# Kernel optimization log

Hardware: AMD Instinct MI355X
Metric: run time of the kernel (lower is better)

## Reference

```python
import jax, jax.numpy as jnp
import numpy as np

B, T, C, H, D, S = 4096, 256, 64, 16, 16, 10


def setup_inputs() -> dict:
    key = jax.random.key(0)
    ks = jax.random.split(key, 8)
    return {
        'states_seq': jax.random.uniform(ks[0], (B, T, S), dtype=jnp.float32) + 0.5,
        'covariates_seq': jax.random.normal(ks[1], (B, T, C), dtype=jnp.float32),
        'ln_gamma': jnp.ones((C,), jnp.float32),
        'ln_beta': jnp.zeros((C,), jnp.float32),
        'rnn_wx': jax.random.normal(ks[2], (C, H), dtype=jnp.float32) * 0.1,
        'rnn_wh': jax.random.normal(ks[3], (H, H), dtype=jnp.float32) * 0.1,
        'rnn_b': jnp.zeros((H,), jnp.float32),
        'd1_w': jax.random.normal(ks[4], (H, H), dtype=jnp.float32) * 0.1,
        'd1_b': jnp.zeros((H,), jnp.float32),
        'd2_w': jax.random.normal(ks[5], (H, D), dtype=jnp.float32) * 0.1,
        'd2_b': jnp.zeros((D,), jnp.float32),
    }


def _cash_budget(s, d):
    # Deterministic cash-budget accounting update.
    # s: (B, 10) = [rev_prev, cash, AR, inventory, PPE, AP, debt, equity, retained, other]
    # d: (B, 16) drivers; first 10 used as ratios.
    sig = jax.nn.sigmoid
    g      = jnp.tanh(d[:, 0]) * 0.2      # sales growth
    cogs_m = sig(d[:, 1])                 # COGS margin
    opex_m = sig(d[:, 2]) * 0.5           # opex margin
    dep_r  = sig(d[:, 3]) * 0.1           # depreciation rate on PPE
    capex_r = sig(d[:, 4]) * 0.2          # capex as % of revenue
    dso = sig(d[:, 5])                    # AR ratio
    dio = sig(d[:, 6])                    # inventory ratio
    dpo = sig(d[:, 7])                    # AP ratio
    tax_r = sig(d[:, 8]) * 0.35           # tax rate
    int_r = sig(d[:, 9]) * 0.1            # interest rate on debt

    rev_prev, cash, ar, inv, ppe, ap, debt, equity, re, other = [s[:, i] for i in range(10)]
    rev = rev_prev * (1.0 + g)
    cogs = cogs_m * rev
    opex = opex_m * rev
    dep = dep_r * ppe
    interest = int_r * debt
    ebt = rev - cogs - opex - dep - interest
    tax = tax_r * jnp.maximum(ebt, 0.0)
    ni = ebt - tax
    ar_new = dso * rev
    inv_new = dio * cogs
    ap_new = dpo * cogs
    capex = capex_r * rev
    ppe_new = ppe + capex - dep
    cash_new = cash + ni + dep - capex - (ar_new - ar) - (inv_new - inv) + (ap_new - ap)
    re_new = re + ni
    s_next = jnp.stack([rev, cash_new, ar_new, inv_new, ppe_new, ap_new, debt, equity, re_new, other], axis=-1)
    is_out = jnp.stack([rev, cogs, opex, dep, interest, tax, ni], axis=-1)  # (B, 7)
    return s_next, is_out


def reference(states_seq, covariates_seq, ln_gamma, ln_beta, rnn_wx, rnn_wh, rnn_b, d1_w, d1_b, d2_w, d2_b):
    # LayerNormalization (keras default eps=1e-3, last axis)
    mu = covariates_seq.mean(-1, keepdims=True)
    var = covariates_seq.var(-1, keepdims=True)
    x = (covariates_seq - mu) * jax.lax.rsqrt(var + 1e-3) * ln_gamma + ln_beta

    # SimpleRNN: h_t = tanh(x_t Wx + h_{t-1} Wh + b), return_sequences
    xw = jnp.einsum('btc,ch->bth', x, rnn_wx) + rnn_b  # precompute input projection

    def rnn_step(h, xt):
        h = jnp.tanh(xt + h @ rnn_wh)
        return h, h

    h0 = jnp.zeros((x.shape[0], rnn_wh.shape[0]), x.dtype)
    _, hs = jax.lax.scan(rnn_step, h0, jnp.swapaxes(xw, 0, 1))  # (T, B, H)
    hs = jnp.swapaxes(hs, 0, 1)  # (B, T, H)

    drivers = jnp.tanh(hs @ d1_w + d1_b) @ d2_w + d2_b  # (B, T, D)

    # Cash-budget recurrence over t = 1 .. T-1
    def cb_step(s_prev, d_t):
        s_next, is_out = _cash_budget(s_prev, d_t)
        return s_next, (s_next, is_out)

    s0 = states_seq[:, 0, :]
    _, (states_tm, is_tm) = jax.lax.scan(cb_step, s0, jnp.swapaxes(drivers[:, 1:, :], 0, 1))
    states_pred = jnp.swapaxes(states_tm, 0, 1)  # (B, T-1, 10)
    is_pred = jnp.swapaxes(is_tm, 0, 1)          # (B, T-1, 7)
    return states_pred, is_pred
```

## Files before the change

### kernel.cpp

```cpp
#include <hip/hip_runtime.h>
#include <hip/hip_fp16.h>

#define NB 4096
#define NT 256
#define NC 64
#define NH 16
#define NS 10
#define NTO 255

__device__ __forceinline__ float fast_rcp(float x){ return __builtin_amdgcn_rcpf(x); }
__device__ __forceinline__ float fast_rsq(float x){ return __builtin_amdgcn_rsqf(x); }
__device__ __forceinline__ float fsig(float x){ return fast_rcp(1.0f + __expf(-x)); }
__device__ __forceinline__ float ftanh(float x){
    float e = __expf(2.0f*x);
    return fmaf(-2.0f, fast_rcp(e + 1.0f), 1.0f);
}

template<int R>
__device__ __forceinline__ float rotf(float x){
    return __int_as_float(__builtin_amdgcn_update_dpp(
        0, __float_as_int(x), 0x120 + R, 0xF, 0xF, true));
}
__device__ __forceinline__ float row_bcast_sum(float x){
    x += rotf<8>(x);
    x += rotf<4>(x);
    x += rotf<2>(x);
    x += rotf<1>(x);
    return x;
}

__global__ __launch_bounds__(256, 4) void xw_kernel(
    const float* __restrict__ cov, const float* __restrict__ lng,
    const float* __restrict__ lnb, const float* __restrict__ wx,
    const float* __restrict__ rnb, __half* __restrict__ xws)
{
    const int wid  = threadIdx.x >> 6;
    const int lane = threadIdx.x & 63;
    const int g = lane >> 4, l = lane & 15;
    const int b = (blockIdx.x << 2) + wid;

    float gwr[64];
    #pragma unroll
    for (int r = 0; r < 16; ++r) {
        int c0 = 4 * ((l - r) & 15);
        #pragma unroll
        for (int j = 0; j < 4; ++j)
            gwr[4*r+j] = lng[c0+j] * wx[(c0+j)*NH + l];
    }
    float bwb = rnb[l];
    #pragma unroll
    for (int c = 0; c < NC; ++c) bwb = fmaf(lnb[c], wx[c*NH + l], bwb);

    const float4* gp = (const float4*)cov + (size_t)b*NT*16 + g*16 + l;
    __half* op = xws + ((size_t)b*16 + l)*NT + g;

    float4 cur = gp[0];
    float4 nxt = gp[64];
    #pragma unroll 2
    for (int it = 0; it < 64; ++it) {
        float4 x = cur;
        cur = nxt;
        if (it < 62) nxt = gp[(size_t)(it+2)*64];
        float ss = (x.x + x.y) + (x.z + x.w);
        float sq = fmaf(x.x,x.x, fmaf(x.y,x.y, fmaf(x.z,x.z, x.w*x.w)));
        ss = row_bcast_sum(ss);
        sq = row_bcast_sum(sq);
        float mu  = ss * (1.0f/64.0f);
        float var = fmaf(-mu, mu, sq * (1.0f/64.0f));
        float rs  = fast_rsq(var + 0.001f);
        float nmu = -mu * rs;
        float x0 = fmaf(x.x, rs, nmu), x1 = fmaf(x.y, rs, nmu);
        float x2 = fmaf(x.z, rs, nmu), x3 = fmaf(x.w, rs, nmu);
        float a0 = bwb, a1 = 0.f, a2 = 0.f, a3 = 0.f;
        a0 = fmaf(x0, gwr[0], a0); a1 = fmaf(x1, gwr[1], a1);
        a2 = fmaf(x2, gwr[2], a2); a3 = fmaf(x3, gwr[3], a3);
#define ROTSTEP(R) { float r0=rotf<R>(x0), r1=rotf<R>(x1), r2=rotf<R>(x2), r3=rotf<R>(x3); \
        a0=fmaf(r0,gwr[4*R+0],a0); a1=fmaf(r1,gwr[4*R+1],a1); \
        a2=fmaf(r2,gwr[4*R+2],a2); a3=fmaf(r3,gwr[4*R+3],a3); }
        ROTSTEP(1)  ROTSTEP(2)  ROTSTEP(3)  ROTSTEP(4)  ROTSTEP(5)
        ROTSTEP(6)  ROTSTEP(7)  ROTSTEP(8)  ROTSTEP(9)  ROTSTEP(10)
        ROTSTEP(11) ROTSTEP(12) ROTSTEP(13) ROTSTEP(14) ROTSTEP(15)
#undef ROTSTEP
        float xw = (a0+a1)+(a2+a3);
        op[it*4] = __float2half(xw);
    }
}

__global__ __launch_bounds__(64, 1) void scan_kernel(
    const float* __restrict__ states, const __half* __restrict__ xws,
    const float* __restrict__ wh,     const float* __restrict__ d1w,
    const float* __restrict__ d1b,    const float* __restrict__ d2w,
    const float* __restrict__ d2b,    float* __restrict__ out)
{
    const int lane = threadIdx.x;
    const int g = lane >> 4, l = lane & 15;
    const int b = (blockIdx.x << 2) + g;

    __shared__ __align__(16) float db[8*64];

    float whr[NH], d1r[NH], d2r[NH];
    #pragma unroll
    for (int r = 0; r < NH; ++r) {
        int src = (l - r) & 15;
        whr[r] = wh[src*NH + l];
        d1r[r] = d1w[src*NH + l];
        d2r[r] = d2w[src*NH + l];
    }
    const float d1bl = d1b[l], d2bl = d2b[l];
    const float Aa = (l==0)?0.4f:(l==2)?0.5f:(l==3)?0.1f:(l==4)?0.2f:(l==8)?0.35f:(l==9)?0.1f:1.0f;
    const float Ba = (l==0)?2.0f:1.0f;
    const float Ca = (l==0)?-0.2f:0.0f;

    float s0,s1,s2,s3,s4,s5,s6,s7,s8,s9;
    { const float* sp = states + (size_t)b*NT*NS;
      s0=sp[0];s1=sp[1];s2=sp[2];s3=sp[3];s4=sp[4];
      s5=sp[5];s6=sp[6];s7=sp[7];s8=sp[8];s9=sp[9]; }

    float* spo = out + (size_t)b*NTO*NS + l;
    float* ipo = out + (size_t)NB*NTO*NS + (size_t)b*NTO*7 + l;

    const ushort4* xp = (const ushort4*)(xws + ((size_t)b*16 + l)*NT);
    ushort4 xa = xp[0], xb = xp[1];

    float h = 0.f;
    float t1p = 0.f;

#define XH(V,U) __half2float(__ushort_as_half((U)==0?(V).x:(U)==1?(V).y:(U)==2?(V).z:(V).w))

#define STEP(J, XWV, S1F, S2F, S3F, S4F) do { \
     \
    float4 w0{}, w1{}; float2 w2{}; \
    if (S4F) { const float* rb = db + ((((J)-3)&7)<<6) + (g<<4); \
        w0 = *(const float4*)rb; w1 = *(const float4*)(rb+4); w2 = *(const float2*)(rb+8); } \
    float hn = h, t1n = t1p; \
    float eR = 0.f, eD = 0.f, sR = 0.f, sD = 0.f; \
    if (S1F || S2F) { \
        float r1=rotf<1>(h),  r2=rotf<2>(h),  r3=rotf<3>(h),  r4=rotf<4>(h); \
        float r5=rotf<5>(h),  r6=rotf<6>(h),  r7=rotf<7>(h),  r8=rotf<8>(h); \
        float r9=rotf<9>(h),  r10=rotf<10>(h), r11=rotf<11>(h), r12=rotf<12>(h); \
        float r13=rotf<13>(h), r14=rotf<14>(h), r15=rotf<15>(h); \
        float aR0=(XWV), aR1=0.f, aR2=0.f, aR3=0.f; \
        float aD0=d1bl,  aD1=0.f, aD2=0.f, aD3=0.f; \
        if (S1F) aR0=fmaf(h,  whr[0], aR0);   if (S2F) aD0=fmaf(h,  d1r[0], aD0); \
        if (S1F) aR1=fmaf(r1, whr[1], aR1);   if (S2F) aD1=fmaf(r1, d1r[1], aD1); \
        if (S1F) aR2=fmaf(r2, whr[2], aR2);   if (S2F) aD2=fmaf(r2, d1r[2], aD2); \
        if (S1F) aR3=fmaf(r3, whr[3], aR3);   if (S2F) aD3=fmaf(r3, d1r[3], aD3); \
        if (S1F) aR0=fmaf(r4, whr[4], aR0);   if (S2F) aD0=fmaf(r4, d1r[4], aD0); \
        if (S1F) aR1=fmaf(r5, whr[5], aR1);   if (S2F) aD1=fmaf(r5, d1r[5], aD1); \
        if (S1F) aR2=fmaf(r6, whr[6], aR2);   if (S2F) aD2=fmaf(r6, d1r[6], aD2); \
        if (S1F) aR3=fmaf(r7, whr[7], aR3);   if (S2F) aD3=fmaf(r7, d1r[7], aD3); \
        if (S1F) aR0=fmaf(r8, whr[8], aR0);   if (S2F) aD0=fmaf(r8, d1r[8], aD0); \
        if (S1F) aR1=fmaf(r9, whr[9], aR1);   if (S2F) aD1=fmaf(r9, d1r[9], aD1); \
        if (S1F) aR2=fmaf(r10,whr[10],aR2);   if (S2F) aD2=fmaf(r10,d1r[10],aD2); \
        if (S1F) aR3=fmaf(r11,whr[11],aR3);   if (S2F) aD3=fmaf(r11,d1r[11],aD3); \
        if (S1F) aR0=fmaf(r12,whr[12],aR0);   if (S2F) aD0=fmaf(r12,d1r[12],aD0); \
        if (S1F) aR1=fmaf(r13,whr[13],aR1);   if (S2F) aD1=fmaf(r13,d1r[13],aD1); \
        if (S1F) aR2=fmaf(r14,whr[14],aR2);   if (S2F) aD2=fmaf(r14,d1r[14],aD2); \
        if (S1F) aR3=fmaf(r15,whr[15],aR3);   if (S2F) aD3=fmaf(r15,d1r[15],aD3); \
        if (S1F) sR = (aR0+aR1)+(aR2+aR3); \
        if (S2F) sD = (aD0+aD1)+(aD2+aD3); \
        if (S1F) eR = __expf(2.0f*sR); \
        if (S2F) eD = __expf(2.0f*sD); \
    } \
     \
    float dv = 0.f; \
    if (S3F) { \
        float q1=rotf<1>(t1p),  q2=rotf<2>(t1p),  q3=rotf<3>(t1p),  q4=rotf<4>(t1p); \
        float q5=rotf<5>(t1p),  q6=rotf<6>(t1p),  q7=rotf<7>(t1p),  q8=rotf<8>(t1p); \
        float q9=rotf<9>(t1p),  q10=rotf<10>(t1p), q11=rotf<11>(t1p), q12=rotf<12>(t1p); \
        float q13=rotf<13>(t1p), q14=rotf<14>(t1p), q15=rotf<15>(t1p); \
        float aS0=d2bl, aS1=0.f, aS2=0.f, aS3=0.f; \
        aS0=fmaf(t1p,d2r[0],aS0); aS1=fmaf(q1, d2r[1], aS1); \
        aS2=fmaf(q2, d2r[2], aS2); aS3=fmaf(q3, d2r[3], aS3); \
        aS0=fmaf(q4, d2r[4], aS0); aS1=fmaf(q5, d2r[5], aS1); \
        aS2=fmaf(q6, d2r[6], aS2); aS3=fmaf(q7, d2r[7], aS3); \
        aS0=fmaf(q8, d2r[8], aS0); aS1=fmaf(q9, d2r[9], aS1); \
        aS2=fmaf(q10,d2r[10],aS2); aS3=fmaf(q11,d2r[11],aS3); \
        aS0=fmaf(q12,d2r[12],aS0); aS1=fmaf(q13,d2r[13],aS1); \
        aS2=fmaf(q14,d2r[14],aS2); aS3=fmaf(q15,d2r[15],aS3); \
        dv = (aS0+aS1)+(aS2+aS3); \
    } \
     \
    if (S1F) hn  = fmaf(-2.0f, fast_rcp(eR+1.0f), 1.0f); \
    if (S2F) t1n = fmaf(-2.0f, fast_rcp(eD+1.0f), 1.0f); \
    if (S3F) { \
        float es = __expf(-Ba*dv); \
        float act = fmaf(Aa, fast_rcp(1.0f+es), Ca); \
        db[((((J)-2)&7)<<6) + lane] = act; \
    } \
    if (S4F) { \
        float rev   = fmaf(s0, w0.x, s0); \
        float cogs  = w0.y * rev; \
        float opex  = w0.z * rev; \
        float dep   = w0.w * s4; \
        float inte  = w2.y * s6; \
        float ebt   = (((rev - cogs) - opex) - dep) - inte; \
        float tax   = w2.x * fmaxf(ebt, 0.0f); \
        float ni    = ebt - tax; \
        float arn   = w1.y * rev; \
        float invn  = w1.z * cogs; \
        float apn   = w1.w * cogs; \
        float capex = w1.x * rev; \
        float ppen  = (s4 + capex) - dep; \
        float cashn = (((((s1 + ni) + dep) - capex) - (arn - s2)) - (invn - s3)) + (apn - s5); \
        float ren   = s8 + ni; \
        s0=rev; s1=cashn; s2=arn; s3=invn; s4=ppen; s5=apn; s8=ren; \
        float sv = (l==0)?rev:(l==1)?cashn:(l==2)?arn:(l==3)?invn:(l==4)?ppen: \
                   (l==5)?apn:(l==6)?s6:(l==7)?s7:(l==8)?ren:s9; \
        float iv = (l==0)?rev:(l==1)?cogs:(l==2)?opex:(l==3)?dep:(l==4)?inte:(l==5)?tax:ni; \
        if (l < NS) *spo = sv; \
        if (l < 7)  *ipo = iv; \
        spo += NS; ipo += 7; \
    } \
    h = hn; t1p = t1n; \
} while(0)

    {
        ushort4 xc = xa; xa = xb; xb = xp[2];
        h = ftanh(XH(xc,0));
        STEP(1, XH(xc,1), 1,0,0,0);
        STEP(2, XH(xc,2), 1,1,0,0);
        STEP(3, XH(xc,3), 1,1,1,0);
    }

    #pragma unroll 1
    for (int tt = 1; tt < 64; ++tt) {
        ushort4 xc = xa; xa = xb;
        if (tt < 62) xb = xp[tt+2];
        STEP(4*tt+0, XH(xc,0), 1,1,1,1);
        STEP(4*tt+1, XH(xc,1), 1,1,1,1);
        STEP(4*tt+2, XH(xc,2), 1,1,1,1);
        STEP(4*tt+3, XH(xc,3), 1,1,1,1);
    }

    STEP(256, 0.0f, 0,1,1,1);
    STEP(257, 0.0f, 0,0,1,1);
    STEP(258, 0.0f, 0,0,0,1);

#undef STEP
#undef XH
}

extern "C" void kernel_launch(void* const* d_in, const int* in_sizes, int n_in,
                              void* d_out, int out_size, void* d_ws, size_t ws_size,
                              hipStream_t stream) {
    (void)in_sizes; (void)n_in; (void)ws_size; (void)out_size;
    __half* xws = (__half*)d_ws;
    xw_kernel<<<NB/4, 256, 0, stream>>>(
        (const float*)d_in[1],
        (const float*)d_in[2],
        (const float*)d_in[3],
        (const float*)d_in[4],
        (const float*)d_in[6],
        xws);
    scan_kernel<<<NB/4, 64, 0, stream>>>(
        (const float*)d_in[0],
        xws,
        (const float*)d_in[5],
        (const float*)d_in[7],
        (const float*)d_in[8],
        (const float*)d_in[9],
        (const float*)d_in[10],
        (float*)d_out);
}
```

Baseline: 583.5 us.

## Split scan into producer and consumer wavefronts linked by a shared-memory ring

The single-wave scan kernel becomes a two-wave block. Wave 0 runs the RNN and driver MLP and writes activations into a 16-slot shared-memory ring. Wave 1 runs the cash-budget recurrence and stores outputs in groups of 8 steps, with a block barrier after each group. This takes the cash-budget arithmetic and global stores off the serial RNN critical path so the two run concurrently, at the cost of per-group barriers and twice the threads per block.

```diff
diff --git a/kernel.cpp b/kernel.cpp
--- a/kernel.cpp
+++ b/kernel.cpp
@@ -10,7 +10,6 @@
 
 __device__ __forceinline__ float fast_rcp(float x){ return __builtin_amdgcn_rcpf(x); }
 __device__ __forceinline__ float fast_rsq(float x){ return __builtin_amdgcn_rsqf(x); }
-__device__ __forceinline__ float fsig(float x){ return fast_rcp(1.0f + __expf(-x)); }
 __device__ __forceinline__ float ftanh(float x){
     float e = __expf(2.0f*x);
     return fmaf(-2.0f, fast_rcp(e + 1.0f), 1.0f);
@@ -86,52 +85,53 @@
     }
 }
 
-__global__ __launch_bounds__(64, 1) void scan_kernel(
+__global__ __launch_bounds__(128, 1) void scan_pc(
     const float* __restrict__ states, const __half* __restrict__ xws,
     const float* __restrict__ wh,     const float* __restrict__ d1w,
     const float* __restrict__ d1b,    const float* __restrict__ d2w,
     const float* __restrict__ d2b,    float* __restrict__ out)
 {
-    const int lane = threadIdx.x;
+    const int tid  = threadIdx.x;
+    const int wid  = tid >> 6;
+    const int lane = tid & 63;
     const int g = lane >> 4, l = lane & 15;
     const int b = (blockIdx.x << 2) + g;
 
-    __shared__ __align__(16) float db[8*64];
+    __shared__ __align__(16) float db[16*64];
 
     float whr[NH], d1r[NH], d2r[NH];
-    #pragma unroll
-    for (int r = 0; r < NH; ++r) {
-        int src = (l - r) & 15;
-        whr[r] = wh[src*NH + l];
-        d1r[r] = d1w[src*NH + l];
-        d2r[r] = d2w[src*NH + l];
-    }
-    const float d1bl = d1b[l], d2bl = d2b[l];
-    const float Aa = (l==0)?0.4f:(l==2)?0.5f:(l==3)?0.1f:(l==4)?0.2f:(l==8)?0.35f:(l==9)?0.1f:1.0f;
-    const float Ba = (l==0)?2.0f:1.0f;
-    const float Ca = (l==0)?-0.2f:0.0f;
-
-    float s0,s1,s2,s3,s4,s5,s6,s7,s8,s9;
-    { const float* sp = states + (size_t)b*NT*NS;
-      s0=sp[0];s1=sp[1];s2=sp[2];s3=sp[3];s4=sp[4];
-      s5=sp[5];s6=sp[6];s7=sp[7];s8=sp[8];s9=sp[9]; }
-
+    float d1bl = 0.f, d2bl = 0.f;
+    float Aa = 1.f, Ba = 1.f, Ca = 0.f;
+    float h = 0.f, t1p = 0.f;
+    const ushort4* xp = (const ushort4*)(xws + ((size_t)b*16 + l)*NT);
+    ushort4 xA{}, xB{}, xC{}, xD{};
+
+    float s0=0,s1=0,s2=0,s3=0,s4=0,s5=0,s6=0,s7=0,s8=0,s9=0;
     float* spo = out + (size_t)b*NTO*NS + l;
     float* ipo = out + (size_t)NB*NTO*NS + (size_t)b*NTO*7 + l;
 
-    const ushort4* xp = (const ushort4*)(xws + ((size_t)b*16 + l)*NT);
-    ushort4 xa = xp[0], xb = xp[1];
-
-    float h = 0.f;
-    float t1p = 0.f;
+    if (wid == 0) {
+        #pragma unroll
+        for (int r = 0; r < NH; ++r) {
+            int src = (l - r) & 15;
+            whr[r] = wh[src*NH + l];
+            d1r[r] = d1w[src*NH + l];
+            d2r[r] = d2w[src*NH + l];
+        }
+        d1bl = d1b[l]; d2bl = d2b[l];
+        Aa = (l==0)?0.4f:(l==2)?0.5f:(l==3)?0.1f:(l==4)?0.2f:(l==8)?0.35f:(l==9)?0.1f:1.0f;
+        Ba = (l==0)?2.0f:1.0f;
+        Ca = (l==0)?-0.2f:0.0f;
+        xA = xp[0]; xB = xp[1]; xC = xp[2]; xD = xp[3];
+    } else {
+        const float* sp = states + (size_t)b*NT*NS;
+        s0=sp[0];s1=sp[1];s2=sp[2];s3=sp[3];s4=sp[4];
+        s5=sp[5];s6=sp[6];s7=sp[7];s8=sp[8];s9=sp[9];
+    }
 
 #define XH(V,U) __half2float(__ushort_as_half((U)==0?(V).x:(U)==1?(V).y:(U)==2?(V).z:(V).w))
 
-#define STEP(J, XWV, S1F, S2F, S3F, S4F) do { \
-     \
-    float4 w0{}, w1{}; float2 w2{}; \
-    if (S4F) { const float* rb = db + ((((J)-3)&7)<<6) + (g<<4); \
-        w0 = *(const float4*)rb; w1 = *(const float4*)(rb+4); w2 = *(const float2*)(rb+8); } \
+#define PSTEP(ACTI, XWV, S1F, S2F, S3F) do { \
     float hn = h, t1n = t1p; \
     float eR = 0.f, eD = 0.f, sR = 0.f, sD = 0.f; \
     if (S1F || S2F) { \
@@ -162,7 +162,6 @@
         if (S1F) eR = __expf(2.0f*sR); \
         if (S2F) eD = __expf(2.0f*sD); \
     } \
-     \
     float dv = 0.f; \
     if (S3F) { \
         float q1=rotf<1>(t1p),  q2=rotf<2>(t1p),  q3=rotf<3>(t1p),  q4=rotf<4>(t1p); \
@@ -180,64 +179,99 @@
         aS2=fmaf(q14,d2r[14],aS2); aS3=fmaf(q15,d2r[15],aS3); \
         dv = (aS0+aS1)+(aS2+aS3); \
     } \
-     \
     if (S1F) hn  = fmaf(-2.0f, fast_rcp(eR+1.0f), 1.0f); \
     if (S2F) t1n = fmaf(-2.0f, fast_rcp(eD+1.0f), 1.0f); \
     if (S3F) { \
         float es = __expf(-Ba*dv); \
         float act = fmaf(Aa, fast_rcp(1.0f+es), Ca); \
-        db[((((J)-2)&7)<<6) + lane] = act; \
-    } \
-    if (S4F) { \
-        float rev   = fmaf(s0, w0.x, s0); \
-        float cogs  = w0.y * rev; \
-        float opex  = w0.z * rev; \
-        float dep   = w0.w * s4; \
-        float inte  = w2.y * s6; \
-        float ebt   = (((rev - cogs) - opex) - dep) - inte; \
-        float tax   = w2.x * fmaxf(ebt, 0.0f); \
-        float ni    = ebt - tax; \
-        float arn   = w1.y * rev; \
-        float invn  = w1.z * cogs; \
-        float apn   = w1.w * cogs; \
-        float capex = w1.x * rev; \
-        float ppen  = (s4 + capex) - dep; \
-        float cashn = (((((s1 + ni) + dep) - capex) - (arn - s2)) - (invn - s3)) + (apn - s5); \
-        float ren   = s8 + ni; \
-        s0=rev; s1=cashn; s2=arn; s3=invn; s4=ppen; s5=apn; s8=ren; \
-        float sv = (l==0)?rev:(l==1)?cashn:(l==2)?arn:(l==3)?invn:(l==4)?ppen: \
-                   (l==5)?apn:(l==6)?s6:(l==7)?s7:(l==8)?ren:s9; \
-        float iv = (l==0)?rev:(l==1)?cogs:(l==2)?opex:(l==3)?dep:(l==4)?inte:(l==5)?tax:ni; \
-        if (l < NS) *spo = sv; \
-        if (l < 7)  *ipo = iv; \
-        spo += NS; ipo += 7; \
+        db[(((ACTI)&15)<<6) + lane] = act; \
     } \
     h = hn; t1p = t1n; \
 } while(0)
 
-    {
-        ushort4 xc = xa; xa = xb; xb = xp[2];
-        h = ftanh(XH(xc,0));
-        STEP(1, XH(xc,1), 1,0,0,0);
-        STEP(2, XH(xc,2), 1,1,0,0);
-        STEP(3, XH(xc,3), 1,1,1,0);
-    }
+#define PGROUP(G) do { \
+    ushort4 x0 = xA, x1 = xB; xA = xC; xB = xD; \
+    if (2*(G)+5 < 64) { xC = xp[2*(G)+4]; xD = xp[2*(G)+5]; } \
+    const int jb = 8*(G); \
+    PSTEP(jb-2, XH(x0,0), 1,1,1); \
+    PSTEP(jb-1, XH(x0,1), 1,1,1); \
+    PSTEP(jb+0, XH(x0,2), 1,1,1); \
+    PSTEP(jb+1, XH(x0,3), 1,1,1); \
+    PSTEP(jb+2, XH(x1,0), 1,1,1); \
+    PSTEP(jb+3, XH(x1,1), 1,1,1); \
+    PSTEP(jb+4, XH(x1,2), 1,1,1); \
+    PSTEP(jb+5, XH(x1,3), 1,1,1); \
+} while(0)
+
+#define CSTEP(T) do { \
+    const float* rb = db + (((T)&15)<<6) + (g<<4); \
+    float4 w0 = *(const float4*)rb; \
+    float4 w1 = *(const float4*)(rb+4); \
+    float2 w2 = *(const float2*)(rb+8); \
+    float rev   = fmaf(s0, w0.x, s0); \
+    float cogs  = w0.y * rev; \
+    float opex  = w0.z * rev; \
+    float dep   = w0.w * s4; \
+    float inte  = w2.y * s6; \
+    float ebt   = (((rev - cogs) - opex) - dep) - inte; \
+    float tax   = w2.x * fmaxf(ebt, 0.0f); \
+    float ni    = ebt - tax; \
+    float arn   = w1.y * rev; \
+    float invn  = w1.z * cogs; \
+    float apn   = w1.w * cogs; \
+    float capex = w1.x * rev; \
+    float ppen  = (s4 + capex) - dep; \
+    float cashn = (((((s1 + ni) + dep) - capex) - (arn - s2)) - (invn - s3)) + (apn - s5); \
+    float ren   = s8 + ni; \
+    s0=rev; s1=cashn; s2=arn; s3=invn; s4=ppen; s5=apn; s8=ren; \
+    float sv = (l==0)?rev:(l==1)?cashn:(l==2)?arn:(l==3)?invn:(l==4)?ppen: \
+               (l==5)?apn:(l==6)?s6:(l==7)?s7:(l==8)?ren:s9; \
+    float iv = (l==0)?rev:(l==1)?cogs:(l==2)?opex:(l==3)?dep:(l==4)?inte:(l==5)?tax:ni; \
+    if (l < NS) *spo = sv; \
+    if (l < 7)  *ipo = iv; \
+    spo += NS; ipo += 7; \
+} while(0)
+
+    if (wid == 0) {
+        ushort4 x0 = xA, x1 = xB; xA = xC; xB = xD;
+        xC = xp[4]; xD = xp[5];
+        h = ftanh(XH(x0,0));
+        PSTEP(0, XH(x0,1), 1,0,0);
+        PSTEP(0, XH(x0,2), 1,1,0);
+        PSTEP(1, XH(x0,3), 1,1,1);
+        PSTEP(2, XH(x1,0), 1,1,1);
+        PSTEP(3, XH(x1,1), 1,1,1);
+        PSTEP(4, XH(x1,2), 1,1,1);
+        PSTEP(5, XH(x1,3), 1,1,1);
+    }
+    __syncthreads();
+
+    if (wid == 0) PGROUP(1);
+    if (wid == 1) { CSTEP(1); CSTEP(2); CSTEP(3); CSTEP(4); CSTEP(5); }
+    __syncthreads();
 
     #pragma unroll 1
-    for (int tt = 1; tt < 64; ++tt) {
-        ushort4 xc = xa; xa = xb;
-        if (tt < 62) xb = xp[tt+2];
-        STEP(4*tt+0, XH(xc,0), 1,1,1,1);
-        STEP(4*tt+1, XH(xc,1), 1,1,1,1);
-        STEP(4*tt+2, XH(xc,2), 1,1,1,1);
-        STEP(4*tt+3, XH(xc,3), 1,1,1,1);
-    }
-
-    STEP(256, 0.0f, 0,1,1,1);
-    STEP(257, 0.0f, 0,0,1,1);
-    STEP(258, 0.0f, 0,0,0,1);
-
-#undef STEP
+    for (int G = 2; G <= 31; ++G) {
+        if (wid == 0) PGROUP(G);
+        if (wid == 1) {
+            const int t0 = 8*G - 10;
+            CSTEP(t0+0); CSTEP(t0+1); CSTEP(t0+2); CSTEP(t0+3);
+            CSTEP(t0+4); CSTEP(t0+5); CSTEP(t0+6); CSTEP(t0+7);
+        }
+        __syncthreads();
+    }
+
+    if (wid == 0) { PSTEP(254, 0.0f, 0,1,1); PSTEP(255, 0.0f, 0,0,1); }
+    if (wid == 1) {
+        CSTEP(246); CSTEP(247); CSTEP(248); CSTEP(249);
+        CSTEP(250); CSTEP(251); CSTEP(252); CSTEP(253);
+    }
+    __syncthreads();
+    if (wid == 1) { CSTEP(254); CSTEP(255); }
+
+#undef CSTEP
+#undef PGROUP
+#undef PSTEP
 #undef XH
 }
 
@@ -253,7 +287,7 @@
         (const float*)d_in[4],
         (const float*)d_in[6],
         xws);
-    scan_kernel<<<NB/4, 64, 0, stream>>>(
+    scan_pc<<<NB/4, 128, 0, stream>>>(
         (const float*)d_in[0],
         xws,
         (const float*)d_in[5],
```

Measured after the change: 565.5 us. 3.1% less time.
